# Kernel tuning notes

Hardware: AMD Instinct MI355X
Metric: run time of the kernel (lower is better)

Reference implementation:

```python
import jax, jax.numpy as jnp
import numpy as np

NEG_SLOPE = 0.2

def gat_conv(x, edge_index, W, a_src, a_dst, b):
    # PyG GATConv, heads=1, eval mode (dropout off), add_self_loops=True
    N = x.shape[0]
    h = x @ W                                   # [N, C]
    loops = jnp.arange(N, dtype=edge_index.dtype)
    src = jnp.concatenate([edge_index[0], loops])
    dst = jnp.concatenate([edge_index[1], loops])
    s_src = h @ a_src                            # [N]
    s_dst = h @ a_dst                            # [N]
    e = s_src[src] + s_dst[dst]                  # [E+N]
    e = jnp.where(e > 0, e, NEG_SLOPE * e)       # leaky_relu
    # segment softmax over destination neighborhoods
    m = jax.ops.segment_max(e, dst, num_segments=N)
    ex = jnp.exp(e - m[dst])
    denom = jax.ops.segment_sum(ex, dst, num_segments=N)
    alpha = ex / denom[dst]                      # [E+N]
    out = jax.ops.segment_sum(alpha[:, None] * h[src], dst, num_segments=N)
    return out + b

def setup_inputs() -> dict:
    key = jax.random.key(0)
    ks = jax.random.split(key, 10)
    N, F_in, H, C, E = 100000, 256, 128, 40, 1600000
    x = jax.random.normal(ks[0], (N, F_in), dtype=jnp.float32)
    edge_index = jax.random.randint(ks[1], (2, E), 0, N, dtype=jnp.int64)
    s1 = 1.0 / np.sqrt(F_in)
    s2 = 1.0 / np.sqrt(H)
    W1 = jax.random.normal(ks[2], (F_in, H), dtype=jnp.float32) * s1
    a_src1 = jax.random.normal(ks[3], (H,), dtype=jnp.float32) * s2
    a_dst1 = jax.random.normal(ks[4], (H,), dtype=jnp.float32) * s2
    b1 = jnp.zeros((H,), dtype=jnp.float32)
    W2 = jax.random.normal(ks[5], (H, C), dtype=jnp.float32) * s2
    a_src2 = jax.random.normal(ks[6], (C,), dtype=jnp.float32) * 0.1
    a_dst2 = jax.random.normal(ks[7], (C,), dtype=jnp.float32) * 0.1
    b2 = jnp.zeros((C,), dtype=jnp.float32)
    return {"x": x, "edge_index": edge_index, "W1": W1, "a_src1": a_src1,
            "a_dst1": a_dst1, "b1": b1, "W2": W2, "a_src2": a_src2,
            "a_dst2": a_dst2, "b2": b2}

def reference(x, edge_index, W1, a_src1, a_dst1, b1, W2, a_src2, a_dst2, b2):
    h = gat_conv(x, edge_index, W1, a_src1, a_dst1, b1)
    h = jax.nn.relu(h)
    # dropout(p=0.6) is identity in eval mode
    h = gat_conv(h, edge_index, W2, a_src2, a_dst2, b2)
    return jax.nn.log_softmax(h, axis=1)
```

## Files before the change

kernel.cpp:

```cpp
#include <hip/hip_runtime.h>
#include <math.h>

#define NEG_SLOPE 0.2f
#define CAP 64
#define NB 64
#define NBUCKET 1563
#define BCAP 1408
#define CHUNK 8192
#define NBINBLK 196

typedef __attribute__((ext_vector_type(8))) short short8;
typedef __attribute__((ext_vector_type(4))) short short4v;
typedef __attribute__((ext_vector_type(4))) float f32x4;
typedef __attribute__((ext_vector_type(2))) float f32x2;

__device__ inline unsigned short f2bf(float f) {
    union { float f; unsigned u; } x; x.f = f;
    unsigned r = x.u + 0x7FFFu + ((x.u >> 16) & 1u);
    return (unsigned short)(r >> 16);
}

__device__ __forceinline__ void gload_lds16(const void* g, void* l) {
    __builtin_amdgcn_global_load_lds(
        (const __attribute__((address_space(1))) void*)g,
        (__attribute__((address_space(3))) void*)l, 16, 0, 0);
}


__global__ __launch_bounds__(256) void front_kernel(
    const int* __restrict__ ei, int* __restrict__ bcnt,
    unsigned* __restrict__ bbuf, int E,
    const float* __restrict__ W1, const float* __restrict__ W2,
    short* __restrict__ bsw1, short* __restrict__ bsw2)
{
    __shared__ int lc[NBUCKET];
    __shared__ int lsrc[CHUNK];
    __shared__ int ldst[CHUNK];
    const int tid = threadIdx.x;

    if (blockIdx.x < NBINBLK) {
        const int base = blockIdx.x * CHUNK;
        const int n = (E - base < CHUNK) ? (E - base) : CHUNK;

        for (int b = tid; b < NBUCKET; b += 256) lc[b] = 0;
        __syncthreads();

        for (int i = tid; i < n; i += 256) {
            int s = ei[base + i];
            int d = ei[E + base + i];
            lsrc[i] = s;
            ldst[i] = d;
            atomicAdd(&lc[d >> 6], 1);
        }
        __syncthreads();

        for (int b = tid; b < NBUCKET; b += 256) {
            int c = lc[b];
            lc[b] = c ? atomicAdd(&bcnt[b], c) : 0;
        }
        __syncthreads();

        for (int i = tid; i < n; i += 256) {
            int s = lsrc[i];
            int d = ldst[i];
            int b = d >> 6;
            int pos = atomicAdd(&lc[b], 1);
            if (pos < BCAP)
                bbuf[(size_t)b * BCAP + pos] = (unsigned)s | ((unsigned)(d & 63) << 17);
        }
    } else {
        int t = (blockIdx.x - NBINBLK) * 256 + tid;
        if (t < 4096) {
            int lane = t & 63;
            int f = t >> 6;
            int k_step = f & 7;
            int n_tile = f >> 3;
            int n  = n_tile * 16 + (lane & 15);
            int k0 = k_step * 32 + (lane >> 4) * 8;
            short8 v;
            #pragma unroll
            for (int j = 0; j < 8; j++)
                v[j] = (short)f2bf(W1[(size_t)(k0 + j) * 128 + n]);
            ((short8*)bsw1)[t] = v;
        } else if (t < 4096 + 768) {
            int u = t - 4096;
            int lane = u & 63;
            int f = u >> 6;
            int k_step = f & 3;
            int n_tile = f >> 2;
            int n  = n_tile * 16 + (lane & 15);
            int k0 = k_step * 32 + (lane >> 4) * 8;
            short8 v;
            #pragma unroll
            for (int j = 0; j < 8; j++)
                v[j] = (n < 40) ? (short)f2bf(W2[(size_t)(k0 + j) * 40 + n]) : (short)0;
            ((short8*)bsw2)[u] = v;
        }
    }
}

__global__ __launch_bounds__(256) void mid_kernel(
    const int* __restrict__ bcnt, const unsigned* __restrict__ bbuf,
    int* __restrict__ csr, int* __restrict__ sorted, int* __restrict__ clsCnt,
    const float* __restrict__ x, const short* __restrict__ bsw,
    const float* __restrict__ a_src, const float* __restrict__ a_dst,
    unsigned char* __restrict__ h1, float* __restrict__ s_src,
    float* __restrict__ s_dst, int M)
{
    __shared__ __align__(16) char smem[16896];
    const int tid = threadIdx.x;

    if (blockIdx.x < NBUCKET) {
        int* lcnt = (int*)smem;
        int (*lcsr)[CAP] = (int(*)[CAP])(smem + 256);
        int* chist = (int*)(smem + 256 + 16384);
        int* cbase = (int*)(smem + 256 + 16384 + 16);

        const int b = blockIdx.x;
        const int nb = b * NB;

        if (tid < NB) lcnt[tid] = 0;
        if (tid < 4) chist[tid] = 0;
        __syncthreads();

        if (tid < NB && nb + tid < M) {
            int pos = atomicAdd(&lcnt[tid], 1);
            if (pos < CAP) lcsr[tid][pos] = nb + tid;
        }

        int ne = bcnt[b]; if (ne > BCAP) ne = BCAP;
        const unsigned* __restrict__ bp = bbuf + (size_t)b * BCAP;
        for (int j = tid; j < ne; j += 256) {
            unsigned v = bp[j];
            int s  = v & 0x1FFFF;
            int dl = v >> 17;
            int pos = atomicAdd(&lcnt[dl], 1);
            if (pos < CAP) lcsr[dl][pos] = s;
        }
        __syncthreads();

        const int4* __restrict__ srcp = (const int4*)&lcsr[0][0];
        int4* __restrict__ dstp = (int4*)(csr + (size_t)nb * CAP);
        #pragma unroll 4
        for (int j = tid; j < NB * CAP / 4; j += 256) dstp[j] = srcp[j];

        int deg = 0, cls = 0, pos = 0;
        bool isNode = (tid < NB && nb + tid < M);
        if (isNode) {
            deg = lcnt[tid]; if (deg > CAP) deg = CAP;
            cls = (deg - 1) >> 4;
            pos = atomicAdd(&chist[cls], 1);
        }
        __syncthreads();
        if (tid < 4) cbase[tid] = chist[tid] ? atomicAdd(&clsCnt[tid], chist[tid]) : 0;
        __syncthreads();
        if (isNode)
            sorted[(size_t)cls * M + cbase[cls] + pos] = (nb + tid) | (deg << 17);
        return;
    }

    const int wave = tid >> 6, lane = tid & 63;
    short8* lbs = (short8*)smem;
    const int rowBase = (blockIdx.x - NBUCKET) * 64;
    const int arow = rowBase + wave * 16 + (lane & 15);
    const int acol0 = (lane >> 4) * 8;
    const bool rv = (arow < M);
    const float* __restrict__ xr = x + (size_t)arow * 256 + acol0;
    const char* __restrict__ bsb = (const char*)bsw;

    auto stage = [&](int buf, int nt) {
        const char* s = bsb + nt * 8192 + wave * 2048 + lane * 16;
        char* d = smem + buf * 8192 + wave * 2048 + lane * 16;
        gload_lds16(s, d);
        gload_lds16(s + 1024, d + 1024);
    };

    stage(0, 0);

    short8 a[8];
    #pragma unroll
    for (int k = 0; k < 8; k++) {
        float4 p = make_float4(0.f, 0.f, 0.f, 0.f);
        float4 q = p;
        if (rv) {
            p = *(const float4*)(xr + k * 32);
            q = *(const float4*)(xr + k * 32 + 4);
        }
        short8 t;
        t[0] = (short)f2bf(p.x); t[1] = (short)f2bf(p.y);
        t[2] = (short)f2bf(p.z); t[3] = (short)f2bf(p.w);
        t[4] = (short)f2bf(q.x); t[5] = (short)f2bf(q.y);
        t[6] = (short)f2bf(q.z); t[7] = (short)f2bf(q.w);
        a[k] = t;
    }

    const int R0 = rowBase + wave * 16 + (lane >> 4) * 4;
    const int Cb = lane & 15;

    float asv[8], adv[8];
    #pragma unroll
    for (int nt = 0; nt < 8; nt++) {
        asv[nt] = a_src[nt * 16 + Cb];
        adv[nt] = a_dst[nt * 16 + Cb];
    }

    stage(1, 1);

    float ss[4] = {0.f, 0.f, 0.f, 0.f};
    float sd[4] = {0.f, 0.f, 0.f, 0.f};
    f32x4 prev = {0.f, 0.f, 0.f, 0.f};
    int wpk[4][4];

    #pragma unroll
    for (int nt = 0; nt < 8; nt++) {
        if (nt == 7) asm volatile("s_waitcnt vmcnt(0)" ::: "memory");
        else         asm volatile("s_waitcnt vmcnt(2)" ::: "memory");
        __builtin_amdgcn_s_barrier();

        short8 breg[8];
        #pragma unroll
        for (int k = 0; k < 8; k++) breg[k] = lbs[(nt & 1) * 512 + k * 64 + lane];
        asm volatile("s_waitcnt lgkmcnt(0)" ::: "memory");
        __builtin_amdgcn_sched_barrier(0);
        __builtin_amdgcn_s_barrier();

        if (nt < 6) stage(nt & 1, nt + 2);

        f32x4 acc = {0.f, 0.f, 0.f, 0.f};
        #pragma unroll
        for (int k = 0; k < 8; k++)
            acc = __builtin_amdgcn_mfma_f32_16x16x32_bf16(a[k], breg[k], acc, 0, 0, 0);

        float as_ = asv[nt], ad_ = adv[nt];
        #pragma unroll
        for (int r = 0; r < 4; r++) {
            float v = acc[r];
            ss[r] = fmaf(v, as_, ss[r]);
            sd[r] = fmaf(v, ad_, sd[r]);
        }
        if (nt & 1) {
            #pragma unroll
            for (int r = 0; r < 4; r++)
                wpk[nt >> 1][r] = __builtin_amdgcn_cvt_pk_fp8_f32(prev[r], acc[r], 0, false);
        } else {
            prev = acc;
        }
    }

    #pragma unroll
    for (int r = 0; r < 4; r++) {
        int R = R0 + r;
        if (R < M) {
            #pragma unroll
            for (int t = 0; t < 4; t++)
                *(unsigned short*)(h1 + (size_t)R * 128 + t * 32 + 2 * Cb) =
                    (unsigned short)wpk[t][r];
        }
    }
    #pragma unroll
    for (int off = 1; off < 16; off <<= 1) {
        #pragma unroll
        for (int r = 0; r < 4; r++) {
            ss[r] += __shfl_xor(ss[r], off);
            sd[r] += __shfl_xor(sd[r], off);
        }
    }
    if ((lane & 15) == 0) {
        #pragma unroll
        for (int r = 0; r < 4; r++) {
            int R = R0 + r;
            if (R < M) { s_src[R] = ss[r]; s_dst[R] = sd[r]; }
        }
    }
}

__global__ __launch_bounds__(256) void agg1_kernel(
    const unsigned char* __restrict__ h, const int* __restrict__ csr,
    const int* __restrict__ sorted, const int* __restrict__ clsCnt,
    const float* __restrict__ s_src, const float* __restrict__ s_dst,
    const float* __restrict__ bias,
    const short* __restrict__ bsw2,
    const float* __restrict__ a_src2, const float* __restrict__ a_dst2,
    unsigned char* __restrict__ h2, float* __restrict__ ss2,
    float* __restrict__ sd2, int N)
{
    __shared__ short lrow[16][136];
    __shared__ int   lnode[16];
    const int tid = threadIdx.x;
    const int lane = tid & 63;
    const int c = lane & 15;
    const int base = lane & 48;
    const int grp = tid >> 4;
    const int g = blockIdx.x * 16 + grp;

    int c0 = clsCnt[0], c01 = c0 + clsCnt[1], c012 = c01 + clsCnt[2];
    int cls, local;
    if (g < c0)        { cls = 0; local = g; }
    else if (g < c01)  { cls = 1; local = g - c0; }
    else if (g < c012) { cls = 2; local = g - c01; }
    else               { cls = 3; local = g - c012; }

    int ent = sorted[(size_t)cls * N + local];
    int n = ent & 0x1FFFF;
    int deg = ent >> 17;
    const int* __restrict__ edges = csr + (size_t)n * CAP;
    float sdn = s_dst[n];

    int s0 = 0, s1 = 0, s2 = 0, s3 = 0;
    float e0 = -1e30f, e1 = -1e30f, e2 = -1e30f, e3 = -1e30f;
    if (c < deg)      { s0 = edges[c];      e0 = s_src[s0] + sdn; }
    if (c + 16 < deg) { s1 = edges[c + 16]; e1 = s_src[s1] + sdn; }
    if (c + 32 < deg) { s2 = edges[c + 32]; e2 = s_src[s2] + sdn; }
    if (c + 48 < deg) { s3 = edges[c + 48]; e3 = s_src[s3] + sdn; }
    e0 = e0 > 0.f ? e0 : NEG_SLOPE * e0;
    e1 = e1 > 0.f ? e1 : NEG_SLOPE * e1;
    e2 = e2 > 0.f ? e2 : NEG_SLOPE * e2;
    e3 = e3 > 0.f ? e3 : NEG_SLOPE * e3;
    float m = fmaxf(fmaxf(e0, e1), fmaxf(e2, e3));
    #pragma unroll
    for (int off = 1; off < 16; off <<= 1) m = fmaxf(m, __shfl_xor(m, off));
    float w0 = (c < deg)      ? __expf(e0 - m) : 0.f;
    float w1 = (c + 16 < deg) ? __expf(e1 - m) : 0.f;
    float w2 = (c + 32 < deg) ? __expf(e2 - m) : 0.f;
    float w3 = (c + 48 < deg) ? __expf(e3 - m) : 0.f;
    float denom = (w0 + w1) + (w2 + w3);
    #pragma unroll
    for (int off = 1; off < 16; off <<= 1) denom += __shfl_xor(denom, off);
    float inv = 1.0f / denom;

    const uint2* __restrict__ hp = (const uint2*)h;
    f32x2 acc0 = {0.f, 0.f}, acc1 = {0.f, 0.f}, acc2 = {0.f, 0.f}, acc3 = {0.f, 0.f};

#define AGG1_BLK(K, SK, WK)                                                  \
    if (16 * K < deg) {                                                      \
        _Pragma("unroll")                                                    \
        for (int jj = 0; jj < 16; jj++) {                                    \
            int   sv = __shfl(SK, base + jj);                                \
            float wv = __shfl(WK, base + jj);                                \
            if (16 * K + jj < deg) {                                         \
                uint2 u = hp[(size_t)sv * 16 + c];                           \
                f32x2 p;                                                     \
                p = __builtin_amdgcn_cvt_pk_f32_fp8(u.x, false); acc0 += p * wv; \
                p = __builtin_amdgcn_cvt_pk_f32_fp8(u.x, true);  acc1 += p * wv; \
                p = __builtin_amdgcn_cvt_pk_f32_fp8(u.y, false); acc2 += p * wv; \
                p = __builtin_amdgcn_cvt_pk_f32_fp8(u.y, true);  acc3 += p * wv; \
            }                                                                \
        }                                                                    \
    }
    AGG1_BLK(0, s0, w0)
    AGG1_BLK(1, s1, w1)
    AGG1_BLK(2, s2, w2)
    AGG1_BLK(3, s3, w3)
#undef AGG1_BLK

    int cA = 32 * (c >> 2) + 4 * (c & 3);
    float4 bA = *(const float4*)&bias[cA];
    float4 bB = *(const float4*)&bias[cA + 16];
    float r0 = fmaxf(fmaf(acc0.x, inv, bA.x), 0.f);
    float r1 = fmaxf(fmaf(acc1.x, inv, bA.y), 0.f);
    float r2 = fmaxf(fmaf(acc2.x, inv, bA.z), 0.f);
    float r3 = fmaxf(fmaf(acc3.x, inv, bA.w), 0.f);
    float q0 = fmaxf(fmaf(acc0.y, inv, bB.x), 0.f);
    float q1 = fmaxf(fmaf(acc1.y, inv, bB.y), 0.f);
    float q2 = fmaxf(fmaf(acc2.y, inv, bB.z), 0.f);
    float q3 = fmaxf(fmaf(acc3.y, inv, bB.w), 0.f);
    short4v oA = { (short)f2bf(r0), (short)f2bf(r1), (short)f2bf(r2), (short)f2bf(r3) };
    short4v oB = { (short)f2bf(q0), (short)f2bf(q1), (short)f2bf(q2), (short)f2bf(q3) };
    *(short4v*)&lrow[grp][cA] = oA;
    *(short4v*)&lrow[grp][cA + 16] = oB;
    if (c == 0) lnode[grp] = n;
    __syncthreads();

    if (tid >= 64) return;

    const short8* __restrict__ bs = (const short8*)bsw2;
    short8 a[4];
    #pragma unroll
    for (int k = 0; k < 4; k++)
        a[k] = *(const short8*)&lrow[lane & 15][(lane >> 4) * 8 + k * 32];

    float accs[3][4];
    float ssv[4] = {0.f, 0.f, 0.f, 0.f};
    float sdv[4] = {0.f, 0.f, 0.f, 0.f};

    #pragma unroll
    for (int nt = 0; nt < 3; nt++) {
        f32x4 acc = {0.f, 0.f, 0.f, 0.f};
        #pragma unroll
        for (int k = 0; k < 4; k++) {
            short8 b = bs[(nt * 4 + k) * 64 + lane];
            acc = __builtin_amdgcn_mfma_f32_16x16x32_bf16(a[k], b, acc, 0, 0, 0);
        }
        int C = nt * 16 + c;
        bool valid = (C < 40);
        float as_ = valid ? a_src2[C] : 0.f;
        float ad_ = valid ? a_dst2[C] : 0.f;
        #pragma unroll
        for (int r = 0; r < 4; r++) {
            float v = acc[r];
            accs[nt][r] = v;
            ssv[r] = fmaf(v, as_, ssv[r]);
            sdv[r] = fmaf(v, ad_, sdv[r]);
        }
    }
    #pragma unroll
    for (int r = 0; r < 4; r++) {
        int node = lnode[(lane >> 4) * 4 + r];
        int wA = __builtin_amdgcn_cvt_pk_fp8_f32(accs[0][r], accs[1][r], 0, false);
        int wB = __builtin_amdgcn_cvt_pk_fp8_f32(accs[2][r], 0.f, 0, false);
        *(unsigned short*)(h2 + (size_t)node * 64 + 2 * c) = (unsigned short)wA;
        *(unsigned short*)(h2 + (size_t)node * 64 + 32 + 2 * c) = (unsigned short)wB;
    }
    #pragma unroll
    for (int off = 1; off < 16; off <<= 1) {
        #pragma unroll
        for (int r = 0; r < 4; r++) {
            ssv[r] += __shfl_xor(ssv[r], off);
            sdv[r] += __shfl_xor(sdv[r], off);
        }
    }
    if (c == 0) {
        #pragma unroll
        for (int r = 0; r < 4; r++) {
            int node = lnode[(lane >> 4) * 4 + r];
            ss2[node] = ssv[r];
            sd2[node] = sdv[r];
        }
    }
}

__global__ __launch_bounds__(256) void agg2_kernel(
    const unsigned char* __restrict__ h, const int* __restrict__ csr,
    const int* __restrict__ sorted, const int* __restrict__ clsCnt,
    const float* __restrict__ s_src, const float* __restrict__ s_dst,
    const float* __restrict__ bias, float* __restrict__ out, int N)
{
    const int lane = threadIdx.x & 63;
    const int c = lane & 15;
    const int base = lane & 48;
    const int g = blockIdx.x * 16 + (threadIdx.x >> 4);

    int c0 = clsCnt[0], c01 = c0 + clsCnt[1], c012 = c01 + clsCnt[2];
    int cls, local;
    if (g < c0)        { cls = 0; local = g; }
    else if (g < c01)  { cls = 1; local = g - c0; }
    else if (g < c012) { cls = 2; local = g - c01; }
    else               { cls = 3; local = g - c012; }

    int ent = sorted[(size_t)cls * N + local];
    int n = ent & 0x1FFFF;
    int deg = ent >> 17;
    const int* __restrict__ edges = csr + (size_t)n * CAP;
    float sdn = s_dst[n];

    int s0 = 0, s1 = 0, s2 = 0, s3 = 0;
    float e0 = -1e30f, e1 = -1e30f, e2 = -1e30f, e3 = -1e30f;
    if (c < deg)      { s0 = edges[c];      e0 = s_src[s0] + sdn; }
    if (c + 16 < deg) { s1 = edges[c + 16]; e1 = s_src[s1] + sdn; }
    if (c + 32 < deg) { s2 = edges[c + 32]; e2 = s_src[s2] + sdn; }
    if (c + 48 < deg) { s3 = edges[c + 48]; e3 = s_src[s3] + sdn; }
    e0 = e0 > 0.f ? e0 : NEG_SLOPE * e0;
    e1 = e1 > 0.f ? e1 : NEG_SLOPE * e1;
    e2 = e2 > 0.f ? e2 : NEG_SLOPE * e2;
    e3 = e3 > 0.f ? e3 : NEG_SLOPE * e3;
    float m = fmaxf(fmaxf(e0, e1), fmaxf(e2, e3));
    #pragma unroll
    for (int off = 1; off < 16; off <<= 1) m = fmaxf(m, __shfl_xor(m, off));
    float w0 = (c < deg)      ? __expf(e0 - m) : 0.f;
    float w1 = (c + 16 < deg) ? __expf(e1 - m) : 0.f;
    float w2 = (c + 32 < deg) ? __expf(e2 - m) : 0.f;
    float w3 = (c + 48 < deg) ? __expf(e3 - m) : 0.f;
    float denom = (w0 + w1) + (w2 + w3);
    #pragma unroll
    for (int off = 1; off < 16; off <<= 1) denom += __shfl_xor(denom, off);
    float inv = 1.0f / denom;

    const unsigned* __restrict__ hp = (const unsigned*)h;
    f32x2 acc0 = {0.f, 0.f}, acc1 = {0.f, 0.f};

#define AGG2_BLK(K, SK, WK)                                                  \
    if (16 * K < deg) {                                                      \
        _Pragma("unroll")                                                    \
        for (int jj = 0; jj < 16; jj++) {                                    \
            int   sv = __shfl(SK, base + jj);                                \
            float wv = __shfl(WK, base + jj);                                \
            if (16 * K + jj < deg) {                                         \
                unsigned u = hp[(size_t)sv * 16 + c];                        \
                f32x2 p;                                                     \
                p = __builtin_amdgcn_cvt_pk_f32_fp8(u, false); acc0 += p * wv; \
                p = __builtin_amdgcn_cvt_pk_f32_fp8(u, true);  acc1 += p * wv; \
            }                                                                \
        }                                                                    \
    }
    AGG2_BLK(0, s0, w0)
    AGG2_BLK(1, s1, w1)
    AGG2_BLK(2, s2, w2)
    AGG2_BLK(3, s3, w3)
#undef AGG2_BLK

    float v0 = -1e30f, v1 = -1e30f, v2 = -1e30f, v3 = -1e30f;
    bool has01 = (c < 8), has0 = (c < 12);
    if (has01) {
        v0 = fmaf(acc0.x, inv, bias[2*c]);
        v1 = fmaf(acc0.y, inv, bias[2*c + 16]);
        v2 = fmaf(acc1.x, inv, bias[2*c + 1]);
        v3 = fmaf(acc1.y, inv, bias[2*c + 17]);
    } else if (has0) {
        v0 = fmaf(acc0.x, inv, bias[2*c + 16]);
        v2 = fmaf(acc1.x, inv, bias[2*c + 17]);
    }

    float mx = fmaxf(fmaxf(v0, v1), fmaxf(v2, v3));
    #pragma unroll
    for (int off = 1; off < 16; off <<= 1) mx = fmaxf(mx, __shfl_xor(mx, off));
    float sum = 0.f;
    if (has01) sum = __expf(v0 - mx) + __expf(v1 - mx) + __expf(v2 - mx) + __expf(v3 - mx);
    else if (has0) sum = __expf(v0 - mx) + __expf(v2 - mx);
    #pragma unroll
    for (int off = 1; off < 16; off <<= 1) sum += __shfl_xor(sum, off);
    float lg = mx + __logf(sum);

    if (has01) {
        *(float2*)&out[(size_t)n * 40 + 2*c]      = make_float2(v0 - lg, v2 - lg);
        *(float2*)&out[(size_t)n * 40 + 2*c + 16] = make_float2(v1 - lg, v3 - lg);
    } else if (has0) {
        *(float2*)&out[(size_t)n * 40 + 2*c + 16] = make_float2(v0 - lg, v2 - lg);
    }
}

extern "C" void kernel_launch(void* const* d_in, const int* in_sizes, int n_in,
                              void* d_out, int out_size, void* d_ws, size_t ws_size,
                              hipStream_t stream)
{
    const float* x      = (const float*)d_in[0];
    const int*   ei     = (const int*)d_in[1];
    const float* W1     = (const float*)d_in[2];
    const float* a_src1 = (const float*)d_in[3];
    const float* a_dst1 = (const float*)d_in[4];
    const float* b1     = (const float*)d_in[5];
    const float* W2     = (const float*)d_in[6];
    const float* a_src2 = (const float*)d_in[7];
    const float* a_dst2 = (const float*)d_in[8];
    const float* b2     = (const float*)d_in[9];
    float* out = (float*)d_out;

    const int N = 100000;
    const int E = 1600000;

    char* ws = (char*)d_ws;
    size_t off = 0;
    auto alloc = [&](size_t bytes) -> void* {
        void* p = ws + off;
        off += (bytes + 255) & ~(size_t)255;
        return p;
    };
    unsigned char*  h1b  = (unsigned char*)alloc((size_t)N * 128);
    unsigned char*  h2b  = (unsigned char*)alloc((size_t)N * 64);
    int*   csr    = (int*)alloc((size_t)NBUCKET * NB * CAP * 4);
    int*   sorted = (int*)alloc((size_t)4 * N * 4);
    float* ss1  = (float*)alloc((size_t)N * 4);
    float* sd1  = (float*)alloc((size_t)N * 4);
    float* ss2  = (float*)alloc((size_t)N * 4);
    float* sd2  = (float*)alloc((size_t)N * 4);
    short* bsw1 = (short*)alloc((size_t)4096 * 8 * 2);
    short* bsw2 = (short*)alloc((size_t)768 * 8 * 2);
    int*   bcnt = (int*)alloc((size_t)(NBUCKET + 4) * 4);
    int*   clsCnt = bcnt + NBUCKET;
    unsigned* bbuf = (unsigned*)alloc((size_t)NBUCKET * BCAP * 4);

    hipMemsetAsync(bcnt, 0, (size_t)(NBUCKET + 4) * 4, stream);

    front_kernel<<<dim3(NBINBLK + 19), dim3(256), 0, stream>>>(
        ei, bcnt, bbuf, E, W1, W2, bsw1, bsw2);

    mid_kernel<<<dim3(NBUCKET + (N + 63) / 64), dim3(256), 0, stream>>>(
        bcnt, bbuf, csr, sorted, clsCnt,
        x, bsw1, a_src1, a_dst1, h1b, ss1, sd1, N);

    agg1_kernel<<<dim3(N / 16), dim3(256), 0, stream>>>(
        h1b, csr, sorted, clsCnt, ss1, sd1, b1,
        bsw2, a_src2, a_dst2, h2b, ss2, sd2, N);

    agg2_kernel<<<dim3(N / 16), dim3(256), 0, stream>>>(
        h2b, csr, sorted, clsCnt, ss2, sd2, b2, out, N);
}
```

Measured before the change: 339.2 us.

## Build per-bucket CSR in LDS inside aggregation kernels, drop global CSR and degree sort

Edge binning moves into the GEMM kernel, so binning and the first-layer projection run concurrently in one launch, and the W packing becomes its own tiny kernel. Each aggregation kernel now processes one 64-node bucket per block and rebuilds that bucket's adjacency lists in shared memory from the binned edge buffer. This removes the global CSR write and read and the degree-class sorting pass. The cost is that both aggregation kernels redo the LDS CSR build, each block uses more LDS (about 34KB), and without degree sorting the nodes within a block have uneven degrees, which can hurt load balance.

```diff
diff --git a/kernel.cpp b/kernel.cpp
--- a/kernel.cpp
+++ b/kernel.cpp
@@ -27,81 +27,42 @@
 }
 
 
-__global__ __launch_bounds__(256) void front_kernel(
-    const int* __restrict__ ei, int* __restrict__ bcnt,
-    unsigned* __restrict__ bbuf, int E,
+__global__ __launch_bounds__(256) void pack_kernel(
     const float* __restrict__ W1, const float* __restrict__ W2,
     short* __restrict__ bsw1, short* __restrict__ bsw2)
 {
-    __shared__ int lc[NBUCKET];
-    __shared__ int lsrc[CHUNK];
-    __shared__ int ldst[CHUNK];
-    const int tid = threadIdx.x;
-
-    if (blockIdx.x < NBINBLK) {
-        const int base = blockIdx.x * CHUNK;
-        const int n = (E - base < CHUNK) ? (E - base) : CHUNK;
-
-        for (int b = tid; b < NBUCKET; b += 256) lc[b] = 0;
-        __syncthreads();
-
-        for (int i = tid; i < n; i += 256) {
-            int s = ei[base + i];
-            int d = ei[E + base + i];
-            lsrc[i] = s;
-            ldst[i] = d;
-            atomicAdd(&lc[d >> 6], 1);
-        }
-        __syncthreads();
-
-        for (int b = tid; b < NBUCKET; b += 256) {
-            int c = lc[b];
-            lc[b] = c ? atomicAdd(&bcnt[b], c) : 0;
-        }
-        __syncthreads();
-
-        for (int i = tid; i < n; i += 256) {
-            int s = lsrc[i];
-            int d = ldst[i];
-            int b = d >> 6;
-            int pos = atomicAdd(&lc[b], 1);
-            if (pos < BCAP)
-                bbuf[(size_t)b * BCAP + pos] = (unsigned)s | ((unsigned)(d & 63) << 17);
-        }
-    } else {
-        int t = (blockIdx.x - NBINBLK) * 256 + tid;
-        if (t < 4096) {
-            int lane = t & 63;
-            int f = t >> 6;
-            int k_step = f & 7;
-            int n_tile = f >> 3;
-            int n  = n_tile * 16 + (lane & 15);
-            int k0 = k_step * 32 + (lane >> 4) * 8;
-            short8 v;
-            #pragma unroll
-            for (int j = 0; j < 8; j++)
-                v[j] = (short)f2bf(W1[(size_t)(k0 + j) * 128 + n]);
-            ((short8*)bsw1)[t] = v;
-        } else if (t < 4096 + 768) {
-            int u = t - 4096;
-            int lane = u & 63;
-            int f = u >> 6;
-            int k_step = f & 3;
-            int n_tile = f >> 2;
-            int n  = n_tile * 16 + (lane & 15);
-            int k0 = k_step * 32 + (lane >> 4) * 8;
-            short8 v;
-            #pragma unroll
-            for (int j = 0; j < 8; j++)
-                v[j] = (n < 40) ? (short)f2bf(W2[(size_t)(k0 + j) * 40 + n]) : (short)0;
-            ((short8*)bsw2)[u] = v;
-        }
+    int t = blockIdx.x * 256 + threadIdx.x;
+    if (t < 4096) {
+        int lane = t & 63;
+        int f = t >> 6;
+        int k_step = f & 7;
+        int n_tile = f >> 3;
+        int n  = n_tile * 16 + (lane & 15);
+        int k0 = k_step * 32 + (lane >> 4) * 8;
+        short8 v;
+        #pragma unroll
+        for (int j = 0; j < 8; j++)
+            v[j] = (short)f2bf(W1[(size_t)(k0 + j) * 128 + n]);
+        ((short8*)bsw1)[t] = v;
+    } else if (t < 4096 + 768) {
+        int u = t - 4096;
+        int lane = u & 63;
+        int f = u >> 6;
+        int k_step = f & 3;
+        int n_tile = f >> 2;
+        int n  = n_tile * 16 + (lane & 15);
+        int k0 = k_step * 32 + (lane >> 4) * 8;
+        short8 v;
+        #pragma unroll
+        for (int j = 0; j < 8; j++)
+            v[j] = (n < 40) ? (short)f2bf(W2[(size_t)(k0 + j) * 40 + n]) : (short)0;
+        ((short8*)bsw2)[u] = v;
     }
 }
 
 __global__ __launch_bounds__(256) void mid_kernel(
-    const int* __restrict__ bcnt, const unsigned* __restrict__ bbuf,
-    int* __restrict__ csr, int* __restrict__ sorted, int* __restrict__ clsCnt,
+    const int* __restrict__ ei, int* __restrict__ bcnt,
+    unsigned* __restrict__ bbuf, int E,
     const float* __restrict__ x, const short* __restrict__ bsw,
     const float* __restrict__ a_src, const float* __restrict__ a_dst,
     unsigned char* __restrict__ h1, float* __restrict__ s_src,
@@ -110,58 +71,40 @@
     __shared__ __align__(16) char smem[16896];
     const int tid = threadIdx.x;
 
-    if (blockIdx.x < NBUCKET) {
-        int* lcnt = (int*)smem;
-        int (*lcsr)[CAP] = (int(*)[CAP])(smem + 256);
-        int* chist = (int*)(smem + 256 + 16384);
-        int* cbase = (int*)(smem + 256 + 16384 + 16);
-
-        const int b = blockIdx.x;
-        const int nb = b * NB;
-
-        if (tid < NB) lcnt[tid] = 0;
-        if (tid < 4) chist[tid] = 0;
+    if (blockIdx.x < NBINBLK) {
+        int* lc = (int*)smem;
+        const int base = blockIdx.x * CHUNK;
+        const int n = (E - base < CHUNK) ? (E - base) : CHUNK;
+
+        for (int b = tid; b < NBUCKET; b += 256) lc[b] = 0;
         __syncthreads();
 
-        if (tid < NB && nb + tid < M) {
-            int pos = atomicAdd(&lcnt[tid], 1);
-            if (pos < CAP) lcsr[tid][pos] = nb + tid;
-        }
-
-        int ne = bcnt[b]; if (ne > BCAP) ne = BCAP;
-        const unsigned* __restrict__ bp = bbuf + (size_t)b * BCAP;
-        for (int j = tid; j < ne; j += 256) {
-            unsigned v = bp[j];
-            int s  = v & 0x1FFFF;
-            int dl = v >> 17;
-            int pos = atomicAdd(&lcnt[dl], 1);
-            if (pos < CAP) lcsr[dl][pos] = s;
+        for (int i = tid; i < n; i += 256) {
+            int d = ei[E + base + i];
+            atomicAdd(&lc[d >> 6], 1);
         }
         __syncthreads();
 
-        const int4* __restrict__ srcp = (const int4*)&lcsr[0][0];
-        int4* __restrict__ dstp = (int4*)(csr + (size_t)nb * CAP);
-        #pragma unroll 4
-        for (int j = tid; j < NB * CAP / 4; j += 256) dstp[j] = srcp[j];
-
-        int deg = 0, cls = 0, pos = 0;
-        bool isNode = (tid < NB && nb + tid < M);
-        if (isNode) {
-            deg = lcnt[tid]; if (deg > CAP) deg = CAP;
-            cls = (deg - 1) >> 4;
-            pos = atomicAdd(&chist[cls], 1);
+        for (int b = tid; b < NBUCKET; b += 256) {
+            int c = lc[b];
+            lc[b] = c ? atomicAdd(&bcnt[b], c) : 0;
         }
         __syncthreads();
-        if (tid < 4) cbase[tid] = chist[tid] ? atomicAdd(&clsCnt[tid], chist[tid]) : 0;
-        __syncthreads();
-        if (isNode)
-            sorted[(size_t)cls * M + cbase[cls] + pos] = (nb + tid) | (deg << 17);
+
+        for (int i = tid; i < n; i += 256) {
+            int s = ei[base + i];
+            int d = ei[E + base + i];
+            int b = d >> 6;
+            int pos = atomicAdd(&lc[b], 1);
+            if (pos < BCAP)
+                bbuf[(size_t)b * BCAP + pos] = (unsigned)s | ((unsigned)(d & 63) << 17);
+        }
         return;
     }
 
     const int wave = tid >> 6, lane = tid & 63;
     short8* lbs = (short8*)smem;
-    const int rowBase = (blockIdx.x - NBUCKET) * 64;
+    const int rowBase = (blockIdx.x - NBINBLK) * 64;
     const int arow = rowBase + wave * 16 + (lane & 15);
     const int acol0 = (lane >> 4) * 8;
     const bool rv = (arow < M);
@@ -275,8 +218,8 @@
 }
 
 __global__ __launch_bounds__(256) void agg1_kernel(
-    const unsigned char* __restrict__ h, const int* __restrict__ csr,
-    const int* __restrict__ sorted, const int* __restrict__ clsCnt,
+    const int* __restrict__ bcnt, const unsigned* __restrict__ bbuf,
+    const unsigned char* __restrict__ h,
     const float* __restrict__ s_src, const float* __restrict__ s_dst,
     const float* __restrict__ bias,
     const short* __restrict__ bsw2,
@@ -284,100 +227,115 @@
     unsigned char* __restrict__ h2, float* __restrict__ ss2,
     float* __restrict__ sd2, int N)
 {
-    __shared__ short lrow[16][136];
-    __shared__ int   lnode[16];
+    __shared__ int   lcnt[NB];
+    __shared__ int   lcsr[NB][CAP];
+    __shared__ short lrow[NB][136];
     const int tid = threadIdx.x;
+    const int b = blockIdx.x, nb = b * NB;
+
+    if (tid < NB) {
+        int node = nb + tid;
+        bool v = node < N;
+        lcnt[tid] = v ? 1 : 0;
+        if (v) lcsr[tid][0] = node;
+    }
+    __syncthreads();
+    int ne = bcnt[b]; if (ne > BCAP) ne = BCAP;
+    const unsigned* __restrict__ bp = bbuf + (size_t)b * BCAP;
+    for (int j = tid; j < ne; j += 256) {
+        unsigned v = bp[j];
+        int s  = v & 0x1FFFF;
+        int dl = v >> 17;
+        int pos = atomicAdd(&lcnt[dl], 1);
+        if (pos < CAP) lcsr[dl][pos] = s;
+    }
+    __syncthreads();
+
     const int lane = tid & 63;
     const int c = lane & 15;
     const int base = lane & 48;
     const int grp = tid >> 4;
-    const int g = blockIdx.x * 16 + grp;
-
-    int c0 = clsCnt[0], c01 = c0 + clsCnt[1], c012 = c01 + clsCnt[2];
-    int cls, local;
-    if (g < c0)        { cls = 0; local = g; }
-    else if (g < c01)  { cls = 1; local = g - c0; }
-    else if (g < c012) { cls = 2; local = g - c01; }
-    else               { cls = 3; local = g - c012; }
-
-    int ent = sorted[(size_t)cls * N + local];
-    int n = ent & 0x1FFFF;
-    int deg = ent >> 17;
-    const int* __restrict__ edges = csr + (size_t)n * CAP;
-    float sdn = s_dst[n];
-
-    int s0 = 0, s1 = 0, s2 = 0, s3 = 0;
-    float e0 = -1e30f, e1 = -1e30f, e2 = -1e30f, e3 = -1e30f;
-    if (c < deg)      { s0 = edges[c];      e0 = s_src[s0] + sdn; }
-    if (c + 16 < deg) { s1 = edges[c + 16]; e1 = s_src[s1] + sdn; }
-    if (c + 32 < deg) { s2 = edges[c + 32]; e2 = s_src[s2] + sdn; }
-    if (c + 48 < deg) { s3 = edges[c + 48]; e3 = s_src[s3] + sdn; }
-    e0 = e0 > 0.f ? e0 : NEG_SLOPE * e0;
-    e1 = e1 > 0.f ? e1 : NEG_SLOPE * e1;
-    e2 = e2 > 0.f ? e2 : NEG_SLOPE * e2;
-    e3 = e3 > 0.f ? e3 : NEG_SLOPE * e3;
-    float m = fmaxf(fmaxf(e0, e1), fmaxf(e2, e3));
-    #pragma unroll
-    for (int off = 1; off < 16; off <<= 1) m = fmaxf(m, __shfl_xor(m, off));
-    float w0 = (c < deg)      ? __expf(e0 - m) : 0.f;
-    float w1 = (c + 16 < deg) ? __expf(e1 - m) : 0.f;
-    float w2 = (c + 32 < deg) ? __expf(e2 - m) : 0.f;
-    float w3 = (c + 48 < deg) ? __expf(e3 - m) : 0.f;
-    float denom = (w0 + w1) + (w2 + w3);
-    #pragma unroll
-    for (int off = 1; off < 16; off <<= 1) denom += __shfl_xor(denom, off);
-    float inv = 1.0f / denom;
-
     const uint2* __restrict__ hp = (const uint2*)h;
-    f32x2 acc0 = {0.f, 0.f}, acc1 = {0.f, 0.f}, acc2 = {0.f, 0.f}, acc3 = {0.f, 0.f};
+
+    for (int r = 0; r < 4; r++) {
+        int v = r * 16 + grp;
+        int node = nb + v;
+        if (node < N) {
+            int deg = lcnt[v]; if (deg > CAP) deg = CAP;
+            const int* edges = lcsr[v];
+            float sdn = s_dst[node];
+
+            int s0 = 0, s1 = 0, s2 = 0, s3 = 0;
+            float e0 = -1e30f, e1 = -1e30f, e2 = -1e30f, e3 = -1e30f;
+            if (c < deg)      { s0 = edges[c];      e0 = s_src[s0] + sdn; }
+            if (c + 16 < deg) { s1 = edges[c + 16]; e1 = s_src[s1] + sdn; }
+            if (c + 32 < deg) { s2 = edges[c + 32]; e2 = s_src[s2] + sdn; }
+            if (c + 48 < deg) { s3 = edges[c + 48]; e3 = s_src[s3] + sdn; }
+            e0 = e0 > 0.f ? e0 : NEG_SLOPE * e0;
+            e1 = e1 > 0.f ? e1 : NEG_SLOPE * e1;
+            e2 = e2 > 0.f ? e2 : NEG_SLOPE * e2;
+            e3 = e3 > 0.f ? e3 : NEG_SLOPE * e3;
+            float m = fmaxf(fmaxf(e0, e1), fmaxf(e2, e3));
+            #pragma unroll
+            for (int off = 1; off < 16; off <<= 1) m = fmaxf(m, __shfl_xor(m, off));
+            float w0 = (c < deg)      ? __expf(e0 - m) : 0.f;
+            float w1 = (c + 16 < deg) ? __expf(e1 - m) : 0.f;
+            float w2 = (c + 32 < deg) ? __expf(e2 - m) : 0.f;
+            float w3 = (c + 48 < deg) ? __expf(e3 - m) : 0.f;
+            float denom = (w0 + w1) + (w2 + w3);
+            #pragma unroll
+            for (int off = 1; off < 16; off <<= 1) denom += __shfl_xor(denom, off);
+            float inv = 1.0f / denom;
+
+            f32x2 acc0 = {0.f, 0.f}, acc1 = {0.f, 0.f}, acc2 = {0.f, 0.f}, acc3 = {0.f, 0.f};
 
 #define AGG1_BLK(K, SK, WK)                                                  \
-    if (16 * K < deg) {                                                      \
-        _Pragma("unroll")                                                    \
-        for (int jj = 0; jj < 16; jj++) {                                    \
-            int   sv = __shfl(SK, base + jj);                                \
-            float wv = __shfl(WK, base + jj);                                \
-            if (16 * K + jj < deg) {                                         \
-                uint2 u = hp[(size_t)sv * 16 + c];                           \
-                f32x2 p;                                                     \
-                p = __builtin_amdgcn_cvt_pk_f32_fp8(u.x, false); acc0 += p * wv; \
-                p = __builtin_amdgcn_cvt_pk_f32_fp8(u.x, true);  acc1 += p * wv; \
-                p = __builtin_amdgcn_cvt_pk_f32_fp8(u.y, false); acc2 += p * wv; \
-                p = __builtin_amdgcn_cvt_pk_f32_fp8(u.y, true);  acc3 += p * wv; \
-            }                                                                \
-        }                                                                    \
-    }
-    AGG1_BLK(0, s0, w0)
-    AGG1_BLK(1, s1, w1)
-    AGG1_BLK(2, s2, w2)
-    AGG1_BLK(3, s3, w3)
+            if (16 * K < deg) {                                              \
+                _Pragma("unroll")                                            \
+                for (int jj = 0; jj < 16; jj++) {                            \
+                    int   sv = __shfl(SK, base + jj);                        \
+                    float wv = __shfl(WK, base + jj);                        \
+                    if (16 * K + jj < deg) {                                 \
+                        uint2 u = hp[(size_t)sv * 16 + c];                   \
+                        f32x2 p;                                             \
+                        p = __builtin_amdgcn_cvt_pk_f32_fp8(u.x, false); acc0 += p * wv; \
+                        p = __builtin_amdgcn_cvt_pk_f32_fp8(u.x, true);  acc1 += p * wv; \
+                        p = __builtin_amdgcn_cvt_pk_f32_fp8(u.y, false); acc2 += p * wv; \
+                        p = __builtin_amdgcn_cvt_pk_f32_fp8(u.y, true);  acc3 += p * wv; \
+                    }                                                        \
+                }                                                            \
+            }
+            AGG1_BLK(0, s0, w0)
+            AGG1_BLK(1, s1, w1)
+            AGG1_BLK(2, s2, w2)
+            AGG1_BLK(3, s3, w3)
 #undef AGG1_BLK
 
-    int cA = 32 * (c >> 2) + 4 * (c & 3);
-    float4 bA = *(const float4*)&bias[cA];
-    float4 bB = *(const float4*)&bias[cA + 16];
-    float r0 = fmaxf(fmaf(acc0.x, inv, bA.x), 0.f);
-    float r1 = fmaxf(fmaf(acc1.x, inv, bA.y), 0.f);
-    float r2 = fmaxf(fmaf(acc2.x, inv, bA.z), 0.f);
-    float r3 = fmaxf(fmaf(acc3.x, inv, bA.w), 0.f);
-    float q0 = fmaxf(fmaf(acc0.y, inv, bB.x), 0.f);
-    float q1 = fmaxf(fmaf(acc1.y, inv, bB.y), 0.f);
-    float q2 = fmaxf(fmaf(acc2.y, inv, bB.z), 0.f);
-    float q3 = fmaxf(fmaf(acc3.y, inv, bB.w), 0.f);
-    short4v oA = { (short)f2bf(r0), (short)f2bf(r1), (short)f2bf(r2), (short)f2bf(r3) };
-    short4v oB = { (short)f2bf(q0), (short)f2bf(q1), (short)f2bf(q2), (short)f2bf(q3) };
-    *(short4v*)&lrow[grp][cA] = oA;
-    *(short4v*)&lrow[grp][cA + 16] = oB;
-    if (c == 0) lnode[grp] = n;
+            int cA = 32 * (c >> 2) + 4 * (c & 3);
+            float4 bA = *(const float4*)&bias[cA];
+            float4 bB = *(const float4*)&bias[cA + 16];
+            float r0 = fmaxf(fmaf(acc0.x, inv, bA.x), 0.f);
+            float r1 = fmaxf(fmaf(acc1.x, inv, bA.y), 0.f);
+            float r2 = fmaxf(fmaf(acc2.x, inv, bA.z), 0.f);
+            float r3 = fmaxf(fmaf(acc3.x, inv, bA.w), 0.f);
+            float q0 = fmaxf(fmaf(acc0.y, inv, bB.x), 0.f);
+            float q1 = fmaxf(fmaf(acc1.y, inv, bB.y), 0.f);
+            float q2 = fmaxf(fmaf(acc2.y, inv, bB.z), 0.f);
+            float q3 = fmaxf(fmaf(acc3.y, inv, bB.w), 0.f);
+            short4v oA = { (short)f2bf(r0), (short)f2bf(r1), (short)f2bf(r2), (short)f2bf(r3) };
+            short4v oB = { (short)f2bf(q0), (short)f2bf(q1), (short)f2bf(q2), (short)f2bf(q3) };
+            *(short4v*)&lrow[v][cA] = oA;
+            *(short4v*)&lrow[v][cA + 16] = oB;
+        }
+    }
     __syncthreads();
 
-    if (tid >= 64) return;
-
+    const int w = tid >> 6;
     const short8* __restrict__ bs = (const short8*)bsw2;
     short8 a[4];
     #pragma unroll
     for (int k = 0; k < 4; k++)
-        a[k] = *(const short8*)&lrow[lane & 15][(lane >> 4) * 8 + k * 32];
+        a[k] = *(const short8*)&lrow[w * 16 + (lane & 15)][(lane >> 4) * 8 + k * 32];
 
     float accs[3][4];
     float ssv[4] = {0.f, 0.f, 0.f, 0.f};
@@ -388,8 +346,8 @@
         f32x4 acc = {0.f, 0.f, 0.f, 0.f};
         #pragma unroll
         for (int k = 0; k < 4; k++) {
-            short8 b = bs[(nt * 4 + k) * 64 + lane];
-            acc = __builtin_amdgcn_mfma_f32_16x16x32_bf16(a[k], b, acc, 0, 0, 0);
+            short8 bfrag = bs[(nt * 4 + k) * 64 + lane];
+            acc = __builtin_amdgcn_mfma_f32_16x16x32_bf16(a[k], bfrag, acc, 0, 0, 0);
         }
         int C = nt * 16 + c;
         bool valid = (C < 40);
@@ -403,13 +361,16 @@
             sdv[r] = fmaf(v, ad_, sdv[r]);
         }
     }
+    const int row0 = w * 16 + (lane >> 4) * 4;
     #pragma unroll
     for (int r = 0; r < 4; r++) {
-        int node = lnode[(lane >> 4) * 4 + r];
-        int wA = __builtin_amdgcn_cvt_pk_fp8_f32(accs[0][r], accs[1][r], 0, false);
-        int wB = __builtin_amdgcn_cvt_pk_fp8_f32(accs[2][r], 0.f, 0, false);
-        *(unsigned short*)(h2 + (size_t)node * 64 + 2 * c) = (unsigned short)wA;
-        *(unsigned short*)(h2 + (size_t)node * 64 + 32 + 2 * c) = (unsigned short)wB;
+        int node = nb + row0 + r;
+        if (node < N) {
+            int wA = __builtin_amdgcn_cvt_pk_fp8_f32(accs[0][r], accs[1][r], 0, false);
+            int wB = __builtin_amdgcn_cvt_pk_fp8_f32(accs[2][r], 0.f, 0, false);
+            *(unsigned short*)(h2 + (size_t)node * 64 + 2 * c) = (unsigned short)wA;
+            *(unsigned short*)(h2 + (size_t)node * 64 + 32 + 2 * c) = (unsigned short)wB;
+        }
     }
     #pragma unroll
     for (int off = 1; off < 16; off <<= 1) {
@@ -422,109 +383,128 @@
     if (c == 0) {
         #pragma unroll
         for (int r = 0; r < 4; r++) {
-            int node = lnode[(lane >> 4) * 4 + r];
-            ss2[node] = ssv[r];
-            sd2[node] = sdv[r];
+            int node = nb + row0 + r;
+            if (node < N) { ss2[node] = ssv[r]; sd2[node] = sdv[r]; }
         }
     }
 }
 
 __global__ __launch_bounds__(256) void agg2_kernel(
-    const unsigned char* __restrict__ h, const int* __restrict__ csr,
-    const int* __restrict__ sorted, const int* __restrict__ clsCnt,
+    const int* __restrict__ bcnt, const unsigned* __restrict__ bbuf,
+    const unsigned char* __restrict__ h,
     const float* __restrict__ s_src, const float* __restrict__ s_dst,
     const float* __restrict__ bias, float* __restrict__ out, int N)
 {
-    const int lane = threadIdx.x & 63;
+    __shared__ int lcnt[NB];
+    __shared__ int lcsr[NB][CAP];
+    const int tid = threadIdx.x;
+    const int b = blockIdx.x, nb = b * NB;
+
+    if (tid < NB) {
+        int node = nb + tid;
+        bool v = node < N;
+        lcnt[tid] = v ? 1 : 0;
+        if (v) lcsr[tid][0] = node;
+    }
+    __syncthreads();
+    int ne = bcnt[b]; if (ne > BCAP) ne = BCAP;
+    const unsigned* __restrict__ bp = bbuf + (size_t)b * BCAP;
+    for (int j = tid; j < ne; j += 256) {
+        unsigned v = bp[j];
+        int s  = v & 0x1FFFF;
+        int dl = v >> 17;
+        int pos = atomicAdd(&lcnt[dl], 1);
+        if (pos < CAP) lcsr[dl][pos] = s;
+    }
+    __syncthreads();
+
+    const int lane = tid & 63;
     const int c = lane & 15;
     const int base = lane & 48;
-    const int g = blockIdx.x * 16 + (threadIdx.x >> 4);
-
-    int c0 = clsCnt[0], c01 = c0 + clsCnt[1], c012 = c01 + clsCnt[2];
-    int cls, local;
-    if (g < c0)        { cls = 0; local = g; }
-    else if (g < c01)  { cls = 1; local = g - c0; }
-    else if (g < c012) { cls = 2; local = g - c01; }
-    else               { cls = 3; local = g - c012; }
-
-    int ent = sorted[(size_t)cls * N + local];
-    int n = ent & 0x1FFFF;
-    int deg = ent >> 17;
-    const int* __restrict__ edges = csr + (size_t)n * CAP;
-    float sdn = s_dst[n];
-
-    int s0 = 0, s1 = 0, s2 = 0, s3 = 0;
-    float e0 = -1e30f, e1 = -1e30f, e2 = -1e30f, e3 = -1e30f;
-    if (c < deg)      { s0 = edges[c];      e0 = s_src[s0] + sdn; }
-    if (c + 16 < deg) { s1 = edges[c + 16]; e1 = s_src[s1] + sdn; }
-    if (c + 32 < deg) { s2 = edges[c + 32]; e2 = s_src[s2] + sdn; }
-    if (c + 48 < deg) { s3 = edges[c + 48]; e3 = s_src[s3] + sdn; }
-    e0 = e0 > 0.f ? e0 : NEG_SLOPE * e0;
-    e1 = e1 > 0.f ? e1 : NEG_SLOPE * e1;
-    e2 = e2 > 0.f ? e2 : NEG_SLOPE * e2;
-    e3 = e3 > 0.f ? e3 : NEG_SLOPE * e3;
-    float m = fmaxf(fmaxf(e0, e1), fmaxf(e2, e3));
-    #pragma unroll
-    for (int off = 1; off < 16; off <<= 1) m = fmaxf(m, __shfl_xor(m, off));
-    float w0 = (c < deg)      ? __expf(e0 - m) : 0.f;
-    float w1 = (c + 16 < deg) ? __expf(e1 - m) : 0.f;
-    float w2 = (c + 32 < deg) ? __expf(e2 - m) : 0.f;
-    float w3 = (c + 48 < deg) ? __expf(e3 - m) : 0.f;
-    float denom = (w0 + w1) + (w2 + w3);
-    #pragma unroll
-    for (int off = 1; off < 16; off <<= 1) denom += __shfl_xor(denom, off);
-    float inv = 1.0f / denom;
-
+    const int grp = tid >> 4;
     const unsigned* __restrict__ hp = (const unsigned*)h;
-    f32x2 acc0 = {0.f, 0.f}, acc1 = {0.f, 0.f};
+
+    for (int r = 0; r < 4; r++) {
+        int v = r * 16 + grp;
+        int node = nb + v;
+        if (node < N) {
+            int deg = lcnt[v]; if (deg > CAP) deg = CAP;
+            const int* edges = lcsr[v];
+            float sdn = s_dst[node];
+
+            int s0 = 0, s1 = 0, s2 = 0, s3 = 0;
+            float e0 = -1e30f, e1 = -1e30f, e2 = -1e30f, e3 = -1e30f;
+            if (c < deg)      { s0 = edges[c];      e0 = s_src[s0] + sdn; }
+            if (c + 16 < deg) { s1 = edges[c + 16]; e1 = s_src[s1] + sdn; }
+            if (c + 32 < deg) { s2 = edges[c + 32]; e2 = s_src[s2] + sdn; }
+            if (c + 48 < deg) { s3 = edges[c + 48]; e3 = s_src[s3] + sdn; }
+            e0 = e0 > 0.f ? e0 : NEG_SLOPE * e0;
+            e1 = e1 > 0.f ? e1 : NEG_SLOPE * e1;
+            e2 = e2 > 0.f ? e2 : NEG_SLOPE * e2;
+            e3 = e3 > 0.f ? e3 : NEG_SLOPE * e3;
+            float m = fmaxf(fmaxf(e0, e1), fmaxf(e2, e3));
+            #pragma unroll
+            for (int off = 1; off < 16; off <<= 1) m = fmaxf(m, __shfl_xor(m, off));
+            float w0 = (c < deg)      ? __expf(e0 - m) : 0.f;
+            float w1 = (c + 16 < deg) ? __expf(e1 - m) : 0.f;
+            float w2 = (c + 32 < deg) ? __expf(e2 - m) : 0.f;
+            float w3 = (c + 48 < deg) ? __expf(e3 - m) : 0.f;
+            float denom = (w0 + w1) + (w2 + w3);
+            #pragma unroll
+            for (int off = 1; off < 16; off <<= 1) denom += __shfl_xor(denom, off);
+            float inv = 1.0f / denom;
+
+            f32x2 acc0 = {0.f, 0.f}, acc1 = {0.f, 0.f};
 
 #define AGG2_BLK(K, SK, WK)                                                  \
-    if (16 * K < deg) {                                                      \
-        _Pragma("unroll")                                                    \
-        for (int jj = 0; jj < 16; jj++) {                                    \
-            int   sv = __shfl(SK, base + jj);                                \
-            float wv = __shfl(WK, base + jj);                                \
-            if (16 * K + jj < deg) {                                         \
-                unsigned u = hp[(size_t)sv * 16 + c];                        \
-                f32x2 p;                                                     \
-                p = __builtin_amdgcn_cvt_pk_f32_fp8(u, false); acc0 += p * wv; \
-                p = __builtin_amdgcn_cvt_pk_f32_fp8(u, true);  acc1 += p * wv; \
-            }                                                                \
-        }                                                                    \
-    }
-    AGG2_BLK(0, s0, w0)
-    AGG2_BLK(1, s1, w1)
-    AGG2_BLK(2, s2, w2)
-    AGG2_BLK(3, s3, w3)
+            if (16 * K < deg) {                                              \
+                _Pragma("unroll")                                            \
+                for (int jj = 0; jj < 16; jj++) {                            \
+                    int   sv = __shfl(SK, base + jj);                        \
+                    float wv = __shfl(WK, base + jj);                        \
+                    if (16 * K + jj < deg) {                                 \
+                        unsigned u = hp[(size_t)sv * 16 + c];                \
+                        f32x2 p;                                             \
+                        p = __builtin_amdgcn_cvt_pk_f32_fp8(u, false); acc0 += p * wv; \
+                        p = __builtin_amdgcn_cvt_pk_f32_fp8(u, true);  acc1 += p * wv; \
+                    }                                                        \
+                }                                                            \
+            }
+            AGG2_BLK(0, s0, w0)
+            AGG2_BLK(1, s1, w1)
+            AGG2_BLK(2, s2, w2)
+            AGG2_BLK(3, s3, w3)
 #undef AGG2_BLK
 
-    float v0 = -1e30f, v1 = -1e30f, v2 = -1e30f, v3 = -1e30f;
-    bool has01 = (c < 8), has0 = (c < 12);
-    if (has01) {
-        v0 = fmaf(acc0.x, inv, bias[2*c]);
-        v1 = fmaf(acc0.y, inv, bias[2*c + 16]);
-        v2 = fmaf(acc1.x, inv, bias[2*c + 1]);
-        v3 = fmaf(acc1.y, inv, bias[2*c + 17]);
-    } else if (has0) {
-        v0 = fmaf(acc0.x, inv, bias[2*c + 16]);
-        v2 = fmaf(acc1.x, inv, bias[2*c + 17]);
-    }
-
-    float mx = fmaxf(fmaxf(v0, v1), fmaxf(v2, v3));
-    #pragma unroll
-    for (int off = 1; off < 16; off <<= 1) mx = fmaxf(mx, __shfl_xor(mx, off));
-    float sum = 0.f;
-    if (has01) sum = __expf(v0 - mx) + __expf(v1 - mx) + __expf(v2 - mx) + __expf(v3 - mx);
-    else if (has0) sum = __expf(v0 - mx) + __expf(v2 - mx);
-    #pragma unroll
-    for (int off = 1; off < 16; off <<= 1) sum += __shfl_xor(sum, off);
-    float lg = mx + __logf(sum);
-
-    if (has01) {
-        *(float2*)&out[(size_t)n * 40 + 2*c]      = make_float2(v0 - lg, v2 - lg);
-        *(float2*)&out[(size_t)n * 40 + 2*c + 16] = make_float2(v1 - lg, v3 - lg);
-    } else if (has0) {
-        *(float2*)&out[(size_t)n * 40 + 2*c + 16] = make_float2(v0 - lg, v2 - lg);
+            float v0 = -1e30f, v1 = -1e30f, v2 = -1e30f, v3 = -1e30f;
+            bool has01 = (c < 8), has0 = (c < 12);
+            if (has01) {
+                v0 = fmaf(acc0.x, inv, bias[2*c]);
+                v1 = fmaf(acc0.y, inv, bias[2*c + 16]);
+                v2 = fmaf(acc1.x, inv, bias[2*c + 1]);
+                v3 = fmaf(acc1.y, inv, bias[2*c + 17]);
+            } else if (has0) {
+                v0 = fmaf(acc0.x, inv, bias[2*c + 16]);
+                v2 = fmaf(acc1.x, inv, bias[2*c + 17]);
+            }
+
+            float mx = fmaxf(fmaxf(v0, v1), fmaxf(v2, v3));
+            #pragma unroll
+            for (int off = 1; off < 16; off <<= 1) mx = fmaxf(mx, __shfl_xor(mx, off));
+            float sum = 0.f;
+            if (has01) sum = __expf(v0 - mx) + __expf(v1 - mx) + __expf(v2 - mx) + __expf(v3 - mx);
+            else if (has0) sum = __expf(v0 - mx) + __expf(v2 - mx);
+            #pragma unroll
+            for (int off = 1; off < 16; off <<= 1) sum += __shfl_xor(sum, off);
+            float lg = mx + __logf(sum);
+
+            if (has01) {
+                *(float2*)&out[(size_t)node * 40 + 2*c]      = make_float2(v0 - lg, v2 - lg);
+                *(float2*)&out[(size_t)node * 40 + 2*c + 16] = make_float2(v1 - lg, v3 - lg);
+            } else if (has0) {
+                *(float2*)&out[(size_t)node * 40 + 2*c + 16] = make_float2(v0 - lg, v2 - lg);
+            }
+        }
     }
 }
 
@@ -556,31 +536,27 @@
     };
     unsigned char*  h1b  = (unsigned char*)alloc((size_t)N * 128);
     unsigned char*  h2b  = (unsigned char*)alloc((size_t)N * 64);
-    int*   csr    = (int*)alloc((size_t)NBUCKET * NB * CAP * 4);
-    int*   sorted = (int*)alloc((size_t)4 * N * 4);
     float* ss1  = (float*)alloc((size_t)N * 4);
     float* sd1  = (float*)alloc((size_t)N * 4);
     float* ss2  = (float*)alloc((size_t)N * 4);
     float* sd2  = (float*)alloc((size_t)N * 4);
     short* bsw1 = (short*)alloc((size_t)4096 * 8 * 2);
     short* bsw2 = (short*)alloc((size_t)768 * 8 * 2);
-    int*   bcnt = (int*)alloc((size_t)(NBUCKET + 4) * 4);
-    int*   clsCnt = bcnt + NBUCKET;
+    int*   bcnt = (int*)alloc((size_t)NBUCKET * 4);
     unsigned* bbuf = (unsigned*)alloc((size_t)NBUCKET * BCAP * 4);
 
-    hipMemsetAsync(bcnt, 0, (size_t)(NBUCKET + 4) * 4, stream);
-
-    front_kernel<<<dim3(NBINBLK + 19), dim3(256), 0, stream>>>(
-        ei, bcnt, bbuf, E, W1, W2, bsw1, bsw2);
-
-    mid_kernel<<<dim3(NBUCKET + (N + 63) / 64), dim3(256), 0, stream>>>(
-        bcnt, bbuf, csr, sorted, clsCnt,
+    hipMemsetAsync(bcnt, 0, (size_t)NBUCKET * 4, stream);
+
+    pack_kernel<<<dim3(19), dim3(256), 0, stream>>>(W1, W2, bsw1, bsw2);
+
+    mid_kernel<<<dim3(NBINBLK + (N + 63) / 64), dim3(256), 0, stream>>>(
+        ei, bcnt, bbuf, E,
         x, bsw1, a_src1, a_dst1, h1b, ss1, sd1, N);
 
-    agg1_kernel<<<dim3(N / 16), dim3(256), 0, stream>>>(
-        h1b, csr, sorted, clsCnt, ss1, sd1, b1,
+    agg1_kernel<<<dim3(NBUCKET), dim3(256), 0, stream>>>(
+        bcnt, bbuf, h1b, ss1, sd1, b1,
         bsw2, a_src2, a_dst2, h2b, ss2, sd2, N);
 
-    agg2_kernel<<<dim3(N / 16), dim3(256), 0, stream>>>(
-        h2b, csr, sorted, clsCnt, ss2, sd2, b2, out, N);
-}
+    agg2_kernel<<<dim3(NBUCKET), dim3(256), 0, stream>>>(
+        bcnt, bbuf, h2b, ss2, sd2, b2, out, N);
+}
```

After: 369.9 us. 9.0% more time.
